# Optimization experiments

Hardware: AMD Instinct MI355X
Metric: run time of the kernel (lower is better)

The kernel has to match this reference:

```python
import jax, jax.numpy as jnp
import numpy as np

TEMPERATURE = 0.5
EPS = 1e-8  # torch.nn.CosineSimilarity default eps


def setup_inputs() -> dict:
    key = jax.random.key(0)
    k1, k2 = jax.random.split(key)
    B, D = 4096, 256
    z1 = jax.random.normal(k1, (B, D), dtype=jnp.float32)
    # z2 = perturbed view of z1 so positive cosine sims are positive
    # (original torch code takes log of the RAW cosine sim, which is NaN
    #  for negative positives; realistic SimCLR positives are correlated views)
    z2 = z1 + 0.1 * jax.random.normal(k2, (B, D), dtype=jnp.float32)
    return {"z1": z1, "z2": z2}


def reference(z1, z2):
    B = z1.shape[0]
    z = jnp.concatenate([z1, z2], axis=0)                      # [2B, D]
    norm = jnp.maximum(jnp.linalg.norm(z, axis=-1, keepdims=True), EPS)
    zn = z / norm
    sim = zn @ zn.T                                            # [2B, 2B] cosine sims
    # positives: sim[i, i+B] and sim[i+B, i] (RAW cosine, per original code)
    pos = jnp.concatenate([jnp.diagonal(sim, offset=B),
                           jnp.diagonal(sim, offset=-B)])      # [2B]
    # mask self-similarity diagonal to -inf before exp-sum
    diag = jnp.eye(2 * B, dtype=bool)
    sim_masked = jnp.where(diag, -jnp.inf, sim)
    denom = jnp.sum(jnp.exp(sim_masked / TEMPERATURE), axis=-1)  # [2B]
    loss = -jnp.mean(jnp.log(pos / denom))
    return loss
```

## Files before the change

### kernel.cpp

```cpp
#include <hip/hip_runtime.h>
#include <hip/hip_bf16.h>


#define NROWS 8192
#define BHALF 4096
#define DDIM  256

typedef __attribute__((ext_vector_type(4))) int   i32x4;
typedef __attribute__((ext_vector_type(8))) int   i32x8;
typedef __attribute__((ext_vector_type(4))) float f32x4;

#define SCALE1 0x7F7F7F7F
#define TWO_LOG2E 2.8853900817779268f

__device__ __forceinline__ void load_lds16(const unsigned char* g, unsigned char* l) {
    __builtin_amdgcn_global_load_lds(
        (const __attribute__((address_space(1))) void*)g,
        (__attribute__((address_space(3))) void*)l, 16, 0, 0);
}

__global__ __launch_bounds__(256) void prep_kernel(const float* __restrict__ z1,
                                                   const float* __restrict__ z2,
                                                   unsigned char* __restrict__ zn8,
                                                   float* __restrict__ posPart,
                                                   float* __restrict__ denom,
                                                   float* __restrict__ out) {
    __shared__ float sp[4];
    int wave = threadIdx.x >> 6;
    int lane = threadIdx.x & 63;
    int i    = blockIdx.x * 4 + wave;
    float4 a = reinterpret_cast<const float4*>(z1 + (size_t)i * DDIM)[lane];
    float4 b = reinterpret_cast<const float4*>(z2 + (size_t)i * DDIM)[lane];
    float ss1 = a.x * a.x + a.y * a.y + a.z * a.z + a.w * a.w;
    float ss2 = b.x * b.x + b.y * b.y + b.z * b.z + b.w * b.w;
    float dd  = a.x * b.x + a.y * b.y + a.z * b.z + a.w * b.w;
    #pragma unroll
    for (int off = 32; off; off >>= 1) {
        ss1 += __shfl_xor(ss1, off);
        ss2 += __shfl_xor(ss2, off);
        dd  += __shfl_xor(dd, off);
    }
    float n1 = fmaxf(sqrtf(ss1), 1e-8f);
    float n2 = fmaxf(sqrtf(ss2), 1e-8f);
    float i1 = 1.0f / n1, i2 = 1.0f / n2;
    int pa = __builtin_amdgcn_cvt_pk_fp8_f32(a.x * i1, a.y * i1, 0, 0);
    pa     = __builtin_amdgcn_cvt_pk_fp8_f32(a.z * i1, a.w * i1, pa, 1);
    int pb = __builtin_amdgcn_cvt_pk_fp8_f32(b.x * i2, b.y * i2, 0, 0);
    pb     = __builtin_amdgcn_cvt_pk_fp8_f32(b.z * i2, b.w * i2, pb, 1);
    reinterpret_cast<int*>(zn8 + (size_t)i * DDIM)[lane] = pa;
    reinterpret_cast<int*>(zn8 + (size_t)(i + BHALF) * DDIM)[lane] = pb;
    if (lane == 0) sp[wave] = __logf(dd * i1 * i2);
    if (threadIdx.x < 8) denom[blockIdx.x * 8 + threadIdx.x] = 0.0f;
    if (blockIdx.x == 0 && threadIdx.x == 64) out[0] = 0.0f;
    __syncthreads();
    if (threadIdx.x == 0)
        posPart[blockIdx.x] = sp[0] + sp[1] + sp[2] + sp[3];
}

__global__ __launch_bounds__(256, 3) void denom_kernel(const unsigned char* __restrict__ zn8,
                                                       float* __restrict__ denom) {
    __shared__ __align__(16) unsigned char sMem[48 * 1024];
    unsigned char* sA  = sMem;
    unsigned char* sB0 = sMem + 32768;
    unsigned char* sB1 = sMem;

    int x = blockIdx.x, y = blockIdx.y;
    int bi, bj;
    if (x > y) { bi = y;      bj = x - 1;  }
    else       { bi = 63 - y; bj = 63 - x; }
    int iBase = bi * 128;
    int jBase = bj * 128;
    bool isDiag = (bi == bj);

    int t    = threadIdx.x;
    int lane = t & 63;
    int wave = t >> 6;
    int col  = lane & 15;
    int quad = lane >> 4;
    int wm = wave >> 1, wn = wave & 1;

    int rowL  = t >> 4;
    int chunk = (t & 15) ^ rowL;

    {
        const unsigned char* gA = zn8 + (size_t)(iBase + rowL) * DDIM + chunk * 16;
        #pragma unroll
        for (int q = 0; q < 8; q++)
            load_lds16(gA + q * 4096, sA + t * 16 + q * 4096);
        const unsigned char* gB = zn8 + (size_t)(jBase + rowL) * DDIM + chunk * 16;
        #pragma unroll
        for (int q = 0; q < 4; q++)
            load_lds16(gB + q * 4096, sB0 + t * 16 + q * 4096);
    }
    __syncthreads();

    i32x8 af[4][2];
    {
        const unsigned char* aRow = sA + (size_t)(wm * 64 + col) * DDIM;
        #pragma unroll
        for (int mt = 0; mt < 4; mt++)
            #pragma unroll
            for (int ks = 0; ks < 2; ks++) {
                int g0 = ks * 8 + quad * 2;
                i32x4 lo = *(const i32x4*)(aRow + mt * 16 * DDIM + ((g0    ) ^ col) * 16);
                i32x4 hi = *(const i32x4*)(aRow + mt * 16 * DDIM + ((g0 + 1) ^ col) * 16);
                af[mt][ks] = __builtin_shufflevector(lo, hi, 0, 1, 2, 3, 4, 5, 6, 7);
            }
    }
    __syncthreads();

    {
        const unsigned char* gB = zn8 + (size_t)(jBase + 64 + rowL) * DDIM + chunk * 16;
        #pragma unroll
        for (int q = 0; q < 4; q++)
            load_lds16(gB + q * 4096, sB1 + t * 16 + q * 4096);
    }

    float rs[4][4];
    #pragma unroll
    for (int mt = 0; mt < 4; mt++)
        #pragma unroll
        for (int r = 0; r < 4; r++) rs[mt][r] = 0.f;

    #pragma unroll
    for (int h = 0; h < 2; h++) {
        if (h) __syncthreads();
        const unsigned char* bRow =
            (h ? sB1 : sB0) + (size_t)(wn * 32 + col) * DDIM;

        i32x8 bfr[2][2];
        #pragma unroll
        for (int nt = 0; nt < 2; nt++)
            #pragma unroll
            for (int ks = 0; ks < 2; ks++) {
                int g0 = ks * 8 + quad * 2;
                i32x4 lo = *(const i32x4*)(bRow + nt * 16 * DDIM + ((g0    ) ^ col) * 16);
                i32x4 hi = *(const i32x4*)(bRow + nt * 16 * DDIM + ((g0 + 1) ^ col) * 16);
                bfr[nt][ks] = __builtin_shufflevector(lo, hi, 0, 1, 2, 3, 4, 5, 6, 7);
            }

        float cs[2] = {0.f, 0.f};
        #pragma unroll
        for (int mt = 0; mt < 4; mt++) {
            int gi = iBase + wm * 64 + mt * 16;
            #pragma unroll
            for (int nt = 0; nt < 2; nt++) {
                f32x4 acc = {0.f, 0.f, 0.f, 0.f};
                acc = __builtin_amdgcn_mfma_scale_f32_16x16x128_f8f6f4(
                          af[mt][0], bfr[nt][0], acc, 0, 0, 0, SCALE1, 0, SCALE1);
                acc = __builtin_amdgcn_mfma_scale_f32_16x16x128_f8f6f4(
                          af[mt][1], bfr[nt][1], acc, 0, 0, 0, SCALE1, 0, SCALE1);
                bool dtile = (gi == jBase + h * 64 + wn * 32 + nt * 16);
                float csl = 0.f;
                #pragma unroll
                for (int r = 0; r < 4; r++) {
                    float e = exp2f(acc[r] * TWO_LOG2E);
                    if (dtile && (quad * 4 + r) == col) e = 0.f;
                    rs[mt][r] += e;
                    csl += e;
                }
                cs[nt] += csl;
            }
        }

        if (!isDiag) {
            #pragma unroll
            for (int nt = 0; nt < 2; nt++) {
                float v = cs[nt];
                v += __shfl_xor(v, 16);
                v += __shfl_xor(v, 32);
                if (quad == 0)
                    atomicAdd(&denom[jBase + h * 64 + wn * 32 + nt * 16 + col], v);
            }
        }
    }

    #pragma unroll
    for (int mt = 0; mt < 4; mt++)
        #pragma unroll
        for (int r = 0; r < 4; r++) {
            float v = rs[mt][r];
            v += __shfl_xor(v, 1);
            v += __shfl_xor(v, 2);
            v += __shfl_xor(v, 4);
            v += __shfl_xor(v, 8);
            rs[mt][r] = v;
        }
    __syncthreads();
    float* red = (float*)(sMem + 16384);
    if (col == 0) {
        #pragma unroll
        for (int mt = 0; mt < 4; mt++)
            #pragma unroll
            for (int r = 0; r < 4; r++)
                red[wn * 128 + wm * 64 + mt * 16 + quad * 4 + r] = rs[mt][r];
    }
    __syncthreads();
    if (t < 128)
        atomicAdd(&denom[iBase + t], red[t] + red[128 + t]);
}

__global__ __launch_bounds__(256) void loss_kernel(const float* __restrict__ posPart,
                                                   const float* __restrict__ denom,
                                                   float* __restrict__ out) {
    __shared__ float sdata[4];
    int t = threadIdx.x;
    float s = __logf(denom[blockIdx.x * 256 + t]);
    if (t < 32) s -= 2.0f * posPart[blockIdx.x * 32 + t];
    #pragma unroll
    for (int off = 32; off; off >>= 1) s += __shfl_xor(s, off);
    if ((t & 63) == 0) sdata[t >> 6] = s;
    __syncthreads();
    if (t == 0)
        atomicAdd(out, (sdata[0] + sdata[1] + sdata[2] + sdata[3]) * (1.0f / NROWS));
}

extern "C" void kernel_launch(void* const* d_in, const int* in_sizes, int n_in,
                              void* d_out, int out_size, void* d_ws, size_t ws_size,
                              hipStream_t stream) {
    const float* z1 = (const float*)d_in[0];
    const float* z2 = (const float*)d_in[1];

    unsigned char* zn8 = (unsigned char*)d_ws;
    float* denom   = (float*)((char*)d_ws + (size_t)NROWS * DDIM);
    float* posPart = denom + NROWS;

    prep_kernel<<<BHALF / 4, 256, 0, stream>>>(z1, z2, zn8, posPart, denom, (float*)d_out);
    denom_kernel<<<dim3(65, 32), 256, 0, stream>>>(zn8, denom);
    loss_kernel<<<NROWS / 256, 256, 0, stream>>>(posPart, denom, (float*)d_out);
}
```

Baseline: 86.31 us.

## Fuse loss reduction into denom kernel via last-block counter; load A fragments directly

The separate loss kernel is removed. Each denom tile block increments a global counter, and the last block to finish reads all denominators with atomic loads and computes the final loss, which saves one kernel launch. The A-operand fragments are now loaded straight from global memory into registers instead of being staged through LDS, which cuts shared memory from 48KB to 32KB and may allow more blocks per CU. The cost is a serial tail: one block does the whole 8192-element reduction. The A loads are also strided global reads with no swizzle.

```diff
diff --git a/kernel.cpp b/kernel.cpp
--- a/kernel.cpp
+++ b/kernel.cpp
@@ -5,6 +5,7 @@
 #define NROWS 8192
 #define BHALF 4096
 #define DDIM  256
+#define NTILE 2080
 
 typedef __attribute__((ext_vector_type(4))) int   i32x4;
 typedef __attribute__((ext_vector_type(8))) int   i32x8;
@@ -24,7 +25,7 @@
                                                    unsigned char* __restrict__ zn8,
                                                    float* __restrict__ posPart,
                                                    float* __restrict__ denom,
-                                                   float* __restrict__ out) {
+                                                   unsigned int* __restrict__ counter) {
     __shared__ float sp[4];
     int wave = threadIdx.x >> 6;
     int lane = threadIdx.x & 63;
@@ -51,18 +52,19 @@
     reinterpret_cast<int*>(zn8 + (size_t)(i + BHALF) * DDIM)[lane] = pb;
     if (lane == 0) sp[wave] = __logf(dd * i1 * i2);
     if (threadIdx.x < 8) denom[blockIdx.x * 8 + threadIdx.x] = 0.0f;
-    if (blockIdx.x == 0 && threadIdx.x == 64) out[0] = 0.0f;
+    if (blockIdx.x == 0 && threadIdx.x == 64) *counter = 0u;
     __syncthreads();
     if (threadIdx.x == 0)
         posPart[blockIdx.x] = sp[0] + sp[1] + sp[2] + sp[3];
 }
 
 __global__ __launch_bounds__(256, 3) void denom_kernel(const unsigned char* __restrict__ zn8,
-                                                       float* __restrict__ denom) {
-    __shared__ __align__(16) unsigned char sMem[48 * 1024];
-    unsigned char* sA  = sMem;
-    unsigned char* sB0 = sMem + 32768;
-    unsigned char* sB1 = sMem;
+                                                       float* __restrict__ denom,
+                                                       const float* __restrict__ posPart,
+                                                       unsigned int* __restrict__ counter,
+                                                       float* __restrict__ out) {
+    __shared__ __align__(16) unsigned char sB[2][64 * DDIM];
+    __shared__ unsigned int sLast;
 
     int x = blockIdx.x, y = blockIdx.y;
     int bi, bj;
@@ -83,28 +85,21 @@
     int chunk = (t & 15) ^ rowL;
 
     {
-        const unsigned char* gA = zn8 + (size_t)(iBase + rowL) * DDIM + chunk * 16;
-        #pragma unroll
-        for (int q = 0; q < 8; q++)
-            load_lds16(gA + q * 4096, sA + t * 16 + q * 4096);
         const unsigned char* gB = zn8 + (size_t)(jBase + rowL) * DDIM + chunk * 16;
         #pragma unroll
         for (int q = 0; q < 4; q++)
-            load_lds16(gB + q * 4096, sB0 + t * 16 + q * 4096);
-    }
-    __syncthreads();
-
+            load_lds16(gB + q * 4096, sB[0] + t * 16 + q * 4096);
+    }
     i32x8 af[4][2];
     {
-        const unsigned char* aRow = sA + (size_t)(wm * 64 + col) * DDIM;
+        const unsigned char* aBase =
+            zn8 + (size_t)(iBase + wm * 64 + col) * DDIM + quad * 32;
         #pragma unroll
         for (int mt = 0; mt < 4; mt++)
             #pragma unroll
             for (int ks = 0; ks < 2; ks++) {
-                int g0 = ks * 8 + quad * 2;
-                i32x4 lo = *(const i32x4*)(aRow + mt * 16 * DDIM + ((g0    ) ^ col) * 16);
-                i32x4 hi = *(const i32x4*)(aRow + mt * 16 * DDIM + ((g0 + 1) ^ col) * 16);
-                af[mt][ks] = __builtin_shufflevector(lo, hi, 0, 1, 2, 3, 4, 5, 6, 7);
+                const i32x4* p = (const i32x4*)(aBase + mt * 16 * DDIM + ks * 128);
+                af[mt][ks] = __builtin_shufflevector(p[0], p[1], 0, 1, 2, 3, 4, 5, 6, 7);
             }
     }
     __syncthreads();
@@ -113,7 +108,7 @@
         const unsigned char* gB = zn8 + (size_t)(jBase + 64 + rowL) * DDIM + chunk * 16;
         #pragma unroll
         for (int q = 0; q < 4; q++)
-            load_lds16(gB + q * 4096, sB1 + t * 16 + q * 4096);
+            load_lds16(gB + q * 4096, sB[1] + t * 16 + q * 4096);
     }
 
     float rs[4][4];
@@ -125,8 +120,7 @@
     #pragma unroll
     for (int h = 0; h < 2; h++) {
         if (h) __syncthreads();
-        const unsigned char* bRow =
-            (h ? sB1 : sB0) + (size_t)(wn * 32 + col) * DDIM;
+        const unsigned char* bRow = sB[h] + (size_t)(wn * 32 + col) * DDIM;
 
         i32x8 bfr[2][2];
         #pragma unroll
@@ -187,7 +181,7 @@
             rs[mt][r] = v;
         }
     __syncthreads();
-    float* red = (float*)(sMem + 16384);
+    float* red = (float*)sB[0];
     if (col == 0) {
         #pragma unroll
         for (int mt = 0; mt < 4; mt++)
@@ -198,21 +192,27 @@
     __syncthreads();
     if (t < 128)
         atomicAdd(&denom[iBase + t], red[t] + red[128 + t]);
-}
-
-__global__ __launch_bounds__(256) void loss_kernel(const float* __restrict__ posPart,
-                                                   const float* __restrict__ denom,
-                                                   float* __restrict__ out) {
-    __shared__ float sdata[4];
-    int t = threadIdx.x;
-    float s = __logf(denom[blockIdx.x * 256 + t]);
-    if (t < 32) s -= 2.0f * posPart[blockIdx.x * 32 + t];
-    #pragma unroll
-    for (int off = 32; off; off >>= 1) s += __shfl_xor(s, off);
-    if ((t & 63) == 0) sdata[t >> 6] = s;
-    __syncthreads();
-    if (t == 0)
-        atomicAdd(out, (sdata[0] + sdata[1] + sdata[2] + sdata[3]) * (1.0f / NROWS));
+
+    __threadfence();
+    if (t == 0) {
+        unsigned int old = atomicAdd(counter, 1u);
+        sLast = (old == NTILE - 1u) ? 1u : 0u;
+    }
+    __syncthreads();
+    if (sLast) {
+        float s = 0.f;
+        for (int i = t; i < NROWS; i += 256)
+            s += __logf(atomicAdd(&denom[i], 0.0f));
+        for (int i = t; i < BHALF / 4; i += 256)
+            s -= 2.0f * posPart[i];
+        #pragma unroll
+        for (int off = 32; off; off >>= 1) s += __shfl_xor(s, off);
+        float* sRed = red;
+        if ((t & 63) == 0) sRed[t >> 6] = s;
+        __syncthreads();
+        if (t == 0)
+            out[0] = (sRed[0] + sRed[1] + sRed[2] + sRed[3]) * (1.0f / NROWS);
+    }
 }
 
 extern "C" void kernel_launch(void* const* d_in, const int* in_sizes, int n_in,
@@ -224,8 +224,9 @@
     unsigned char* zn8 = (unsigned char*)d_ws;
     float* denom   = (float*)((char*)d_ws + (size_t)NROWS * DDIM);
     float* posPart = denom + NROWS;
-
-    prep_kernel<<<BHALF / 4, 256, 0, stream>>>(z1, z2, zn8, posPart, denom, (float*)d_out);
-    denom_kernel<<<dim3(65, 32), 256, 0, stream>>>(zn8, denom);
-    loss_kernel<<<NROWS / 256, 256, 0, stream>>>(posPart, denom, (float*)d_out);
-}
+    unsigned int* counter = (unsigned int*)(posPart + BHALF / 4);
+
+    prep_kernel<<<BHALF / 4, 256, 0, stream>>>(z1, z2, zn8, posPart, denom, counter);
+    denom_kernel<<<dim3(65, 32), 256, 0, stream>>>(zn8, denom, posPart, counter,
+                                                   (float*)d_out);
+}
```

Result: slower. 208.1 us (+141.1%).
